# Optimization experiments

Measured on AMD Instinct MI355X. Metric: run time of the kernel, lower is better.

Reference implementation:

```python
import jax, jax.numpy as jnp
import numpy as np

N, E = 50000, 400000
C_IN, C_OUT = 64, 32
K = 9  # kernel_size 3x3


def _quad_basis(t):
    # open B-spline basis, degree 2, per torch_spline_conv: k_mod in {0,1,2}
    # t = frac(pseudo * (kernel_size - degree)) = pseudo here (kernel_size=3, degree=2)
    return jnp.stack([0.5 * (1.0 - t) ** 2, -t * t + t + 0.5, 0.5 * t * t], axis=-1)  # [E,3]


def spline_basis(pseudo):
    # kernel_size=[3,3], degree=2, open spline: v = p*(3-2)=p, floor(v)=0 for p in [0,1),
    # so weight index for combination s is exactly s = k_mod0 + 3*k_mod1.
    q0 = _quad_basis(pseudo[:, 0])  # [E,3] varies with s%3
    q1 = _quad_basis(pseudo[:, 1])  # [E,3] varies with s//3
    return (q1[:, :, None] * q0[:, None, :]).reshape(-1, K)  # [E,9]


def spline_conv(x, src, dst, B, W, root, bias, n_nodes):
    xj = x[src]  # gather source node features [E,Cin]
    msg = jnp.zeros((xj.shape[0], W.shape[-1]), x.dtype)
    for k in range(K):  # fixed small kernel loop; avoids [E,K,Cin] blowup
        msg = msg + (xj * B[:, k, None]) @ W[k]
    agg = jax.ops.segment_sum(msg, dst, num_segments=n_nodes)  # aggr='add'
    return agg + x @ root + bias


def setup_inputs() -> dict:
    key = jax.random.key(0)
    ks = jax.random.split(key, 10)
    x = jax.random.normal(ks[0], (N, C_IN), jnp.float32)
    edge_index = jax.random.randint(ks[1], (2, E), 0, N, jnp.int64)
    pseudo = jax.random.uniform(ks[2], (E, 2), jnp.float32)
    skip = jax.random.normal(ks[3], (N, C_OUT), jnp.float32)
    s1 = 1.0 / np.sqrt(C_IN)
    s2 = 1.0 / np.sqrt(C_OUT)
    W1 = jax.random.normal(ks[4], (K, C_IN, C_OUT), jnp.float32) * s1
    root1 = jax.random.normal(ks[5], (C_IN, C_OUT), jnp.float32) * s1
    b1 = jnp.zeros((C_OUT,), jnp.float32)
    W2 = jax.random.normal(ks[6], (K, C_OUT, C_OUT), jnp.float32) * s2
    root2 = jax.random.normal(ks[7], (C_OUT, C_OUT), jnp.float32) * s2
    b2 = jnp.zeros((C_OUT,), jnp.float32)
    return {"x": x, "edge_index": edge_index, "pseudo": pseudo, "skip": skip,
            "W1": W1, "root1": root1, "b1": b1, "W2": W2, "root2": root2, "b2": b2}


def reference(x, edge_index, pseudo, skip, W1, root1, b1, W2, root2, b2):
    src, dst = edge_index[0], edge_index[1]  # flow: source_to_target
    B = spline_basis(pseudo)  # [E,9]
    n = x.shape[0]
    h = jax.nn.relu(spline_conv(x, src, dst, B, W1, root1, b1, n))
    h = jnp.concatenate([h, skip], axis=1)  # [N, Cout+Cskip] == [N, Cin]
    h = jax.nn.relu(spline_conv(h, src, dst, B, W1, root1, b1, n))
    h = jax.nn.relu(spline_conv(h, src, dst, B, W2, root2, b2, n))
    return h
```

## Files before the change

kernel.cpp:

```cpp
#include <hip/hip_runtime.h>
#include <hip/hip_bf16.h>


typedef __attribute__((ext_vector_type(8))) short short8;
typedef __attribute__((ext_vector_type(4))) float f32x4;

__device__ __forceinline__ float blo(unsigned u) {
    union { unsigned u; float f; } x; x.u = u << 16; return x.f;
}
__device__ __forceinline__ float bhi(unsigned u) {
    union { unsigned u; float f; } x; x.u = u & 0xffff0000u; return x.f;
}
__device__ __forceinline__ unsigned short f2bf(float f) {
    union { float f; unsigned u; } x; x.f = f;
    unsigned r = x.u + 0x7fffu + ((x.u >> 16) & 1u);
    return (unsigned short)(r >> 16);
}
__device__ __forceinline__ short8 cvt8(const float* p) {
    float4 a = *(const float4*)p;
    float4 b = *(const float4*)(p + 4);
    short8 r;
    r[0] = (short)f2bf(a.x); r[1] = (short)f2bf(a.y);
    r[2] = (short)f2bf(a.z); r[3] = (short)f2bf(a.w);
    r[4] = (short)f2bf(b.x); r[5] = (short)f2bf(b.y);
    r[6] = (short)f2bf(b.z); r[7] = (short)f2bf(b.w);
    return r;
}

#define YROW 296

__device__ __forceinline__ void m_phase(const unsigned short* sY,
                                        const int* __restrict__ sstart,
                                        const float4* __restrict__ erec,
                                        uint4* __restrict__ msgOut,
                                        int n0, int t, int N, int E)
{
    const int e0 = sstart[n0];
    const int e1 = (n0 + 64 < N) ? sstart[n0 + 64] : E;
    const int l  = t & 3;

    for (int e = e0 + (t >> 2); e < e1; e += 64) {
        const float4 r = erec[e];
        const int srcl = __float_as_int(r.x) - n0;
        const int dp   = __float_as_int(r.y);
        const float p0 = r.z, p1 = r.w;

        const float qb[3] = {0.5f * (1.f - p0) * (1.f - p0), -p0 * p0 + p0 + 0.5f, 0.5f * p0 * p0};
        const float qa[3] = {0.5f * (1.f - p1) * (1.f - p1), -p1 * p1 + p1 + 0.5f, 0.5f * p1 * p1};

        const uint4* yb = (const uint4*)(sY + srcl * YROW) + l;
        float s[8] = {0.f, 0.f, 0.f, 0.f, 0.f, 0.f, 0.f, 0.f};
        #pragma unroll
        for (int a = 0; a < 3; ++a) {
            float z[8] = {0.f, 0.f, 0.f, 0.f, 0.f, 0.f, 0.f, 0.f};
            #pragma unroll
            for (int b = 0; b < 3; ++b) {
                uint4 v = yb[(a * 3 + b) * 4];
                const float cw = qb[b];
                z[0] = fmaf(cw, blo(v.x), z[0]); z[1] = fmaf(cw, bhi(v.x), z[1]);
                z[2] = fmaf(cw, blo(v.y), z[2]); z[3] = fmaf(cw, bhi(v.y), z[3]);
                z[4] = fmaf(cw, blo(v.z), z[4]); z[5] = fmaf(cw, bhi(v.z), z[5]);
                z[6] = fmaf(cw, blo(v.w), z[6]); z[7] = fmaf(cw, bhi(v.w), z[7]);
            }
            #pragma unroll
            for (int j = 0; j < 8; ++j) s[j] = fmaf(qa[a], z[j], s[j]);
        }

        union { uint4 u; __hip_bfloat162 h[4]; } o;
        #pragma unroll
        for (int j = 0; j < 4; ++j)
            o.h[j] = __float22bfloat162_rn(float2{s[2 * j], s[2 * j + 1]});
        msgOut[(size_t)dp * 4 + l] = o.u;
    }
}

template<int NHALF>
__device__ __forceinline__ void t_core(short8 a0, short8 a1,
                                       const unsigned short* __restrict__ Wt,
                                       const float* __restrict__ bias,
                                       unsigned short* sY, float* __restrict__ aggOut,
                                       int base, int wv, int lc, int q, int N)
{
    const int CIN = NHALF * 32;
    f32x4 acc[20];
    #pragma unroll
    for (int nt = 0; nt < 20; ++nt) acc[nt] = (f32x4){0.f, 0.f, 0.f, 0.f};

    #pragma unroll
    for (int nt = 0; nt < 20; ++nt) {
        const unsigned short* wp = Wt + ((size_t)(nt * 16 + lc)) * CIN + q * 8;
        acc[nt] = __builtin_amdgcn_mfma_f32_16x16x32_bf16(a0, *(const short8*)wp, acc[nt], 0, 0, 0);
        if (NHALF == 2)
            acc[nt] = __builtin_amdgcn_mfma_f32_16x16x32_bf16(a1, *(const short8*)(wp + 32), acc[nt], 0, 0, 0);
    }

    #pragma unroll
    for (int nt = 0; nt < 18; ++nt) {
        #pragma unroll
        for (int r = 0; r < 4; ++r) {
            int nl = wv * 16 + q * 4 + r;
            sY[nl * YROW + nt * 16 + lc] = f2bf(acc[nt][r]);
        }
    }
    #pragma unroll
    for (int nt = 18; nt < 20; ++nt) {
        int c = (nt - 18) * 16 + lc;
        #pragma unroll
        for (int r = 0; r < 4; ++r) {
            int n = base + q * 4 + r;
            if (n < N) aggOut[(size_t)n * 32 + c] = acc[nt][r] + bias[c];
        }
    }
}

__global__ __launch_bounds__(256)
void layer_tm0(const float* __restrict__ Xa,
               const unsigned short* __restrict__ Wt, const float* __restrict__ bias,
               const int* __restrict__ sstart, const float4* __restrict__ erec,
               float* __restrict__ aggOut, uint4* __restrict__ msgOut, int N, int E)
{
    __shared__ __align__(16) unsigned short sY[64 * YROW];
    const int t = threadIdx.x, wv = t >> 6, lane = t & 63;
    const int lc = lane & 15, q = lane >> 4;
    const int n0 = blockIdx.x * 64, base = n0 + wv * 16;

    int na = base + lc;
    if (na >= N) na = N - 1;
    const float* p = Xa + (size_t)na * 64 + q * 8;
    short8 a0 = cvt8(p);
    short8 a1 = cvt8(p + 32);

    t_core<2>(a0, a1, Wt, bias, sY, aggOut, base, wv, lc, q, N);
    __syncthreads();
    m_phase(sY, sstart, erec, msgOut, n0, t, N, E);
}

template<int MODE>
__global__ __launch_bounds__(256)
void layer_gtm(const float* __restrict__ aggPrev, const float* __restrict__ skipv,
               const unsigned short* __restrict__ Wt, const float* __restrict__ bias,
               const int* __restrict__ sstart, const int* __restrict__ dstart,
               const float4* __restrict__ erec,
               const uint4* __restrict__ msgIn, uint4* __restrict__ msgOut,
               float* __restrict__ aggOut, int N, int E)
{
    __shared__ __align__(16) unsigned short sY[64 * YROW];
    const int t = threadIdx.x, wv = t >> 6, lane = t & 63;
    const int lc = lane & 15, q = lane >> 4;
    const int n0 = blockIdx.x * 64, base = n0 + wv * 16;

    int na = base + lc;
    if (na >= N) na = N - 1;

    const float* ap = aggPrev + (size_t)na * 32 + q * 8;
    float4 r0 = *(const float4*)ap;
    float4 r1 = *(const float4*)(ap + 4);
    float h[8] = {r0.x, r0.y, r0.z, r0.w, r1.x, r1.y, r1.z, r1.w};
    const int ge0 = dstart[na] - E;
    const int ge1 = ((na + 1 < N) ? dstart[na + 1] : 2 * E) - E;
    for (int e = ge0; e < ge1; ++e) {
        uint4 v = msgIn[(size_t)e * 4 + q];
        h[0] += blo(v.x); h[1] += bhi(v.x); h[2] += blo(v.y); h[3] += bhi(v.y);
        h[4] += blo(v.z); h[5] += bhi(v.z); h[6] += blo(v.w); h[7] += bhi(v.w);
    }
    union { short8 v; __hip_bfloat162 h2[4]; } pk;
    #pragma unroll
    for (int j = 0; j < 4; ++j)
        pk.h2[j] = __float22bfloat162_rn(float2{fmaxf(h[2 * j], 0.f), fmaxf(h[2 * j + 1], 0.f)});
    short8 a0 = pk.v;
    short8 a1;
    if (MODE == 1) a1 = cvt8(skipv + (size_t)na * 32 + q * 8);

    t_core<(MODE == 1) ? 2 : 1>(a0, a1, Wt, bias, sY, aggOut, base, wv, lc, q, N);
    __syncthreads();
    m_phase(sY, sstart, erec, msgOut, n0, t, N, E);
}

__global__ __launch_bounds__(256)
void gather_kernel(const int* __restrict__ dstart, const uint4* __restrict__ msg4,
                   float* __restrict__ agg, int N, int E)
{
    const int t = threadIdx.x;
    const int n = blockIdx.x * 64 + (t >> 2);
    if (n >= N) return;
    const int l = t & 3;

    const int e0 = dstart[n] - E;
    const int e1 = ((n + 1 < N) ? dstart[n + 1] : 2 * E) - E;

    float4* ap = (float4*)(agg + (size_t)n * 32 + l * 8);
    float4 A = ap[0], B = ap[1];
    const uint4* mp = msg4 + l;
    for (int e = e0; e < e1; ++e) {
        uint4 v = mp[(size_t)e * 4];
        A.x += blo(v.x); A.y += bhi(v.x); A.z += blo(v.y); A.w += bhi(v.y);
        B.x += blo(v.z); B.y += bhi(v.z); B.z += blo(v.w); B.w += bhi(v.w);
    }
    A.x = fmaxf(A.x, 0.f); A.y = fmaxf(A.y, 0.f); A.z = fmaxf(A.z, 0.f); A.w = fmaxf(A.w, 0.f);
    B.x = fmaxf(B.x, 0.f); B.y = fmaxf(B.y, 0.f); B.z = fmaxf(B.z, 0.f); B.w = fmaxf(B.w, 0.f);
    ap[0] = A; ap[1] = B;
}


__global__ __launch_bounds__(256)
void init_kernel(int* __restrict__ hist, int n2,
                 const float* __restrict__ W1, const float* __restrict__ root1,
                 const float* __restrict__ W2, const float* __restrict__ root2,
                 unsigned short* __restrict__ Wt1, unsigned short* __restrict__ Wt2)
{
    int i = blockIdx.x * 256 + threadIdx.x;
    if (i < n2) { hist[i] = 0; return; }
    int j = i - n2;
    if (j < 320 * 64) {
        int col = j / 64, k = j % 64;
        float v = (col < 288) ? W1[((size_t)(col >> 5) * 64 + k) * 32 + (col & 31)]
                              : root1[(size_t)k * 32 + (col - 288)];
        Wt1[j] = f2bf(v);
    } else if (j < 320 * 96) {
        int jj = j - 320 * 64;
        int col = jj / 32, k = jj % 32;
        float v = (col < 288) ? W2[((size_t)(col >> 5) * 32 + k) * 32 + (col & 31)]
                              : root2[(size_t)k * 32 + (col - 288)];
        Wt2[jj] = f2bf(v);
    }
}

__global__ __launch_bounds__(256)
void count_rank_kernel(const int* __restrict__ ei, int* __restrict__ hist,
                       uint2* __restrict__ rank, int N, int E)
{
    int e = blockIdx.x * 256 + threadIdx.x;
    if (e >= E) return;
    unsigned rs = atomicAdd(&hist[ei[e]], 1);
    unsigned rd = atomicAdd(&hist[N + ei[E + e]], 1);
    rank[e] = uint2{rs, rd};
}

__global__ __launch_bounds__(1024)
void scan1_kernel(int* __restrict__ hist, int* __restrict__ bsum, int n)
{
    __shared__ int s[1024];
    int tid = threadIdx.x;
    int i = blockIdx.x * 1024 + tid;
    int v = (i < n) ? hist[i] : 0;
    s[tid] = v;
    __syncthreads();
    for (int off = 1; off < 1024; off <<= 1) {
        int add = (tid >= off) ? s[tid - off] : 0;
        __syncthreads();
        s[tid] += add;
        __syncthreads();
    }
    if (i < n) hist[i] = s[tid] - v;
    if (tid == 1023) bsum[blockIdx.x] = s[1023];
}

__global__ __launch_bounds__(1024)
void scan3_kernel(int* __restrict__ hist, const int* __restrict__ bsum, int n)
{
    __shared__ int sred[128];
    int tid = threadIdx.x;
    int b = blockIdx.x;
    if (tid < 128) sred[tid] = (tid < b) ? bsum[tid] : 0;
    __syncthreads();
    for (int off = 64; off > 0; off >>= 1) {
        if (tid < off) sred[tid] += sred[tid + off];
        __syncthreads();
    }
    int pre = sred[0];
    int i = b * 1024 + tid;
    if (i < n) hist[i] += pre;
}

__global__ __launch_bounds__(256)
void scatter_plain_kernel(const int* __restrict__ ei, const float* __restrict__ pseudo,
                          const int* __restrict__ start, const uint2* __restrict__ rank,
                          float4* __restrict__ erec, int N, int E)
{
    int e = blockIdx.x * 256 + threadIdx.x;
    if (e >= E) return;
    int sv = ei[e];
    int dv = ei[E + e];
    uint2 rk = rank[e];
    int ps = start[sv] + (int)rk.x;
    int pd = start[N + dv] + (int)rk.y - E;
    float4 r;
    r.x = __int_as_float(sv);
    r.y = __int_as_float(pd);
    r.z = pseudo[2 * (size_t)e];
    r.w = pseudo[2 * (size_t)e + 1];
    erec[ps] = r;
}

extern "C" void kernel_launch(void* const* d_in, const int* in_sizes, int n_in,
                              void* d_out, int out_size, void* d_ws, size_t ws_size,
                              hipStream_t stream) {
    const float* x      = (const float*)d_in[0];
    const int*   ei     = (const int*)  d_in[1];
    const float* pseudo = (const float*)d_in[2];
    const float* skip   = (const float*)d_in[3];
    const float* W1     = (const float*)d_in[4];
    const float* root1  = (const float*)d_in[5];
    const float* b1     = (const float*)d_in[6];
    const float* W2     = (const float*)d_in[7];
    const float* root2  = (const float*)d_in[8];
    const float* b2     = (const float*)d_in[9];

    const int N = in_sizes[0] / 64;
    const int E = in_sizes[1] / 2;
    float* out = (float*)d_out;

    unsigned short* msgA = (unsigned short*)d_ws;
    unsigned short* msgB = msgA + (size_t)E * 32;
    float*  agg1  = (float*)(msgB + (size_t)E * 32);
    float*  agg2  = agg1 + (size_t)N * 32;
    float4* erec  = (float4*)(agg2 + (size_t)N * 32);
    int*    start = (int*)(erec + E);
    int*    bsum  = start + 2 * N;
    unsigned short* Wt1 = (unsigned short*)(bsum + 256);
    unsigned short* Wt2 = Wt1 + 320 * 64;
    uint2*  rank  = (uint2*)msgB;

    const dim3 blk(256);
    const int tb   = (N + 63) / 64;
    const int gb   = (N + 63) / 64;
    const int e256 = (E + 255) / 256;
    const int n2k  = (2 * N + 1023) / 1024;
    const int itot = 2 * N + 320 * 96;
    int* dstart = start + N;

    init_kernel<<<(itot + 255) / 256, blk, 0, stream>>>(start, 2 * N, W1, root1, W2, root2, Wt1, Wt2);
    count_rank_kernel<<<e256, blk, 0, stream>>>(ei, start, rank, N, E);
    scan1_kernel<<<n2k, 1024, 0, stream>>>(start, bsum, 2 * N);
    scan3_kernel<<<n2k, 1024, 0, stream>>>(start, bsum, 2 * N);
    scatter_plain_kernel<<<e256, blk, 0, stream>>>(ei, pseudo, start, rank, erec, N, E);

    layer_tm0<<<tb, blk, 0, stream>>>(x, Wt1, b1, start, erec, agg1, (uint4*)msgA, N, E);
    layer_gtm<1><<<tb, blk, 0, stream>>>(agg1, skip, Wt1, b1, start, dstart, erec,
                                         (const uint4*)msgA, (uint4*)msgB, agg2, N, E);
    layer_gtm<2><<<tb, blk, 0, stream>>>(agg2, nullptr, Wt2, b2, start, dstart, erec,
                                         (const uint4*)msgB, (uint4*)msgA, out, N, E);
    gather_kernel<<<gb, blk, 0, stream>>>(dstart, (const uint4*)msgA, out, N, E);
}
```

Before: 264.1 us.

## Halve nodes per block and split MFMA column tiles across wave pairs

The fused transform+message kernels now handle 32 nodes per block instead of 64. Each pair of waves shares a 16-row tile and splits the 20 output column tiles into two groups of 10. This halves the accumulator registers per wave and the shared-memory Y buffer, and doubles the number of blocks, which should raise occupancy and parallelism. The cost is more blocks, each carrying its own per-block edge-range overhead, and each wave loading a second A fragment.

```diff
diff --git a/kernel.cpp b/kernel.cpp
--- a/kernel.cpp
+++ b/kernel.cpp
@@ -36,7 +36,7 @@
                                         int n0, int t, int N, int E)
 {
     const int e0 = sstart[n0];
-    const int e1 = (n0 + 64 < N) ? sstart[n0 + 64] : E;
+    const int e1 = (n0 + 32 < N) ? sstart[n0 + 32] : E;
     const int l  = t & 3;
 
     for (int e = e0 + (t >> 2); e < e1; e += 64) {
@@ -79,36 +79,39 @@
                                        const unsigned short* __restrict__ Wt,
                                        const float* __restrict__ bias,
                                        unsigned short* sY, float* __restrict__ aggOut,
-                                       int base, int wv, int lc, int q, int N)
+                                       int n0, int rh, int cg, int lc, int q, int N)
 {
     const int CIN = NHALF * 32;
-    f32x4 acc[20];
+    f32x4 acc[10];
     #pragma unroll
-    for (int nt = 0; nt < 20; ++nt) acc[nt] = (f32x4){0.f, 0.f, 0.f, 0.f};
+    for (int j = 0; j < 10; ++j) acc[j] = (f32x4){0.f, 0.f, 0.f, 0.f};
 
     #pragma unroll
-    for (int nt = 0; nt < 20; ++nt) {
-        const unsigned short* wp = Wt + ((size_t)(nt * 16 + lc)) * CIN + q * 8;
-        acc[nt] = __builtin_amdgcn_mfma_f32_16x16x32_bf16(a0, *(const short8*)wp, acc[nt], 0, 0, 0);
+    for (int j = 0; j < 10; ++j) {
+        const int ti = cg * 10 + j;
+        const unsigned short* wp = Wt + ((size_t)(ti * 16 + lc)) * CIN + q * 8;
+        acc[j] = __builtin_amdgcn_mfma_f32_16x16x32_bf16(a0, *(const short8*)wp, acc[j], 0, 0, 0);
         if (NHALF == 2)
-            acc[nt] = __builtin_amdgcn_mfma_f32_16x16x32_bf16(a1, *(const short8*)(wp + 32), acc[nt], 0, 0, 0);
+            acc[j] = __builtin_amdgcn_mfma_f32_16x16x32_bf16(a1, *(const short8*)(wp + 32), acc[j], 0, 0, 0);
     }
 
     #pragma unroll
-    for (int nt = 0; nt < 18; ++nt) {
-        #pragma unroll
-        for (int r = 0; r < 4; ++r) {
-            int nl = wv * 16 + q * 4 + r;
-            sY[nl * YROW + nt * 16 + lc] = f2bf(acc[nt][r]);
-        }
-    }
-    #pragma unroll
-    for (int nt = 18; nt < 20; ++nt) {
-        int c = (nt - 18) * 16 + lc;
-        #pragma unroll
-        for (int r = 0; r < 4; ++r) {
-            int n = base + q * 4 + r;
-            if (n < N) aggOut[(size_t)n * 32 + c] = acc[nt][r] + bias[c];
+    for (int j = 0; j < 10; ++j) {
+        const int ti = cg * 10 + j;
+        if (ti < 18) {
+            #pragma unroll
+            for (int r = 0; r < 4; ++r) {
+                int nl = rh * 16 + q * 4 + r;
+                sY[nl * YROW + ti * 16 + lc] = f2bf(acc[j][r]);
+            }
+        } else {
+            int c = (ti - 18) * 16 + lc;
+            float bv = bias[c];
+            #pragma unroll
+            for (int r = 0; r < 4; ++r) {
+                int n = n0 + rh * 16 + q * 4 + r;
+                if (n < N) aggOut[(size_t)n * 32 + c] = acc[j][r] + bv;
+            }
         }
     }
 }
@@ -119,18 +122,19 @@
                const int* __restrict__ sstart, const float4* __restrict__ erec,
                float* __restrict__ aggOut, uint4* __restrict__ msgOut, int N, int E)
 {
-    __shared__ __align__(16) unsigned short sY[64 * YROW];
+    __shared__ __align__(16) unsigned short sY[32 * YROW];
     const int t = threadIdx.x, wv = t >> 6, lane = t & 63;
     const int lc = lane & 15, q = lane >> 4;
-    const int n0 = blockIdx.x * 64, base = n0 + wv * 16;
-
-    int na = base + lc;
+    const int rh = wv & 1, cg = wv >> 1;
+    const int n0 = blockIdx.x * 32;
+
+    int na = n0 + rh * 16 + lc;
     if (na >= N) na = N - 1;
     const float* p = Xa + (size_t)na * 64 + q * 8;
     short8 a0 = cvt8(p);
     short8 a1 = cvt8(p + 32);
 
-    t_core<2>(a0, a1, Wt, bias, sY, aggOut, base, wv, lc, q, N);
+    t_core<2>(a0, a1, Wt, bias, sY, aggOut, n0, rh, cg, lc, q, N);
     __syncthreads();
     m_phase(sY, sstart, erec, msgOut, n0, t, N, E);
 }
@@ -144,12 +148,13 @@
                const uint4* __restrict__ msgIn, uint4* __restrict__ msgOut,
                float* __restrict__ aggOut, int N, int E)
 {
-    __shared__ __align__(16) unsigned short sY[64 * YROW];
+    __shared__ __align__(16) unsigned short sY[32 * YROW];
     const int t = threadIdx.x, wv = t >> 6, lane = t & 63;
     const int lc = lane & 15, q = lane >> 4;
-    const int n0 = blockIdx.x * 64, base = n0 + wv * 16;
-
-    int na = base + lc;
+    const int rh = wv & 1, cg = wv >> 1;
+    const int n0 = blockIdx.x * 32;
+
+    int na = n0 + rh * 16 + lc;
     if (na >= N) na = N - 1;
 
     const float* ap = aggPrev + (size_t)na * 32 + q * 8;
@@ -171,7 +176,7 @@
     short8 a1;
     if (MODE == 1) a1 = cvt8(skipv + (size_t)na * 32 + q * 8);
 
-    t_core<(MODE == 1) ? 2 : 1>(a0, a1, Wt, bias, sY, aggOut, base, wv, lc, q, N);
+    t_core<(MODE == 1) ? 2 : 1>(a0, a1, Wt, bias, sY, aggOut, n0, rh, cg, lc, q, N);
     __syncthreads();
     m_phase(sY, sstart, erec, msgOut, n0, t, N, E);
 }
@@ -322,7 +327,7 @@
     uint2*  rank  = (uint2*)msgB;
 
     const dim3 blk(256);
-    const int tb   = (N + 63) / 64;
+    const int tb   = (N + 31) / 32;
     const int gb   = (N + 63) / 64;
     const int e256 = (E + 255) / 256;
     const int n2k  = (2 * N + 1023) / 1024;
```

New measurement: 251.6 us. -4.7%, faster.
